# Kernel tuning notes

Measured on AMD Instinct MI355X. Metric: run time of the kernel, lower is better.

## Reference

```python
import jax, jax.numpy as jnp
import numpy as np
from jax import lax

B, L, E, H, VOCAB = 32, 64, 1024, 128, 32000


def setup_inputs() -> dict:
    key = jax.random.key(0)
    ks = jax.random.split(key, 8)
    return {
        "sent": jax.random.randint(ks[0], (B, L), 0, VOCAB),
        "init_c": jax.random.normal(ks[1], (B, H), jnp.float32),
        "init_h": jax.random.normal(ks[2], (B, H), jnp.float32),
        "enc_output": jax.random.normal(ks[3], (B, E, H), jnp.float32),
        "w_emb": jax.random.normal(ks[4], (VOCAB, H), jnp.float32) * 0.02,
        "w_lstm": jax.random.normal(ks[5], (2 * H, 4 * H), jnp.float32) * 0.05,
        "w_soft": jax.random.normal(ks[6], (H, VOCAB), jnp.float32) * 0.05,
        "V": jax.random.normal(ks[7], (2 * H, H), jnp.float32) * 0.05,
    }


def reference(sent, init_c, init_h, enc_output, w_emb, w_lstm, w_soft, V):
    h_dim = init_h.shape[-1]
    x_emb = w_emb[sent]                       # (B, L, H) embedding lookup
    # Split additive-attention matrix: concat(enc, h) @ V == enc @ V_e + h @ V_h
    V_e, V_h = V[:h_dim], V[h_dim:]           # (H, H) each
    enc_proj = enc_output @ V_e               # (B, E, H), precomputed once

    def step(carry, x_t):
        c, h = carry
        # LSTM cell: gates from concat(x, h) @ w_lstm
        gates = jnp.concatenate([x_t, h], axis=-1) @ w_lstm   # (B, 4H)
        i, f, o, g = jnp.split(gates, 4, axis=-1)
        c_new = jax.nn.sigmoid(f) * c + jax.nn.sigmoid(i) * jnp.tanh(g)
        h_new = jax.nn.sigmoid(o) * jnp.tanh(c_new)           # (B, H)
        # Bahdanau additive attention over encoder states
        att = jnp.tanh(enc_proj + (h_new @ V_h)[:, None, :])  # (B, E, H)
        scores = att.sum(axis=-1)                              # (B, E)
        alpha = jax.nn.softmax(scores, axis=-1)                # (B, E)
        context = jnp.einsum('be,beh->bh', alpha, enc_output)  # (B, H)
        h_out = context                                        # attended hidden
        return (c_new, h_out), (h_out, alpha)

    (c_fin, h_fin), (hs, alphas) = lax.scan(step, (init_c, init_h),
                                            jnp.transpose(x_emb, (1, 0, 2)))
    hs = jnp.transpose(hs, (1, 0, 2))          # (B, L, H)
    alphas = jnp.transpose(alphas, (1, 0, 2))  # (B, L, E)
    logits = hs @ w_soft                       # (B, L, vocab)
    return logits, c_fin, h_fin, alphas
```

## Files before the change

kernel.cpp:

```cpp
#include <hip/hip_runtime.h>
#include <hip/hip_bf16.h>

#define BB 32
#define LL 64
#define EE 1024
#define HH 128
#define VV 32000

typedef unsigned short u16;
typedef unsigned long long u64;
typedef __attribute__((ext_vector_type(8))) short bf16x8;
typedef __attribute__((ext_vector_type(4))) float f32x4;

#define LOG2E 1.4426950408889634f
#define C2T   2.8853900817779268f

#define OFF_C ((size_t)BB * LL * VV)
#define OFF_H (OFF_C + (size_t)BB * HH)
#define OFF_A (OFF_H + (size_t)BB * HH)

#define WS_ENCT 0
#define WS_HS   ((size_t)16777216)
#define WS_GX   ((size_t)18350080)
#define WS_PAYU ((size_t)22544384)
#define WS_PAYG ((size_t)23076864)
#define WS_DFL  ((size_t)23339008)
#define WS_NEED ((size_t)23339012)

#define PAYU_WORDS (32 * 8 * 2 * 130)
#define PAYG_WORDS (32 * 8 * 2 * 64)
#define PAY_TOTAL  (PAYU_WORDS + PAYG_WORDS)

__device__ __forceinline__ float bf2f(u16 u) {
    union { unsigned int i; float f; } v; v.i = ((unsigned int)u) << 16; return v.f;
}
__device__ __forceinline__ u16 f2bf(float f) {
    union { float f; unsigned int i; } v; v.f = f;
    unsigned int x = v.i;
    return (u16)((x + 0x7FFFu + ((x >> 16) & 1u)) >> 16);
}
__device__ __forceinline__ float ldf(const void* p, size_t i, int f32) {
    if (f32) return ((const float*)p)[i];
    return bf2f(((const u16*)p)[i]);
}
__device__ __forceinline__ void stout(void* p, size_t i, float v, int f32) {
    if (f32) ((float*)p)[i] = v;
    else ((u16*)p)[i] = f2bf(v);
}
__device__ __forceinline__ float sigm(float x) {
    return __builtin_amdgcn_rcpf(1.f + __builtin_amdgcn_exp2f(-x * LOG2E));
}
__device__ __forceinline__ float tanh_fast(float x) {
    return 1.f - 2.f * __builtin_amdgcn_rcpf(__builtin_amdgcn_exp2f(x * C2T) + 1.f);
}

__global__ __launch_bounds__(256) void resetdetect_kernel(
    u64* __restrict__ pay, const unsigned int* __restrict__ w, int* __restrict__ flag)
{
    int i = blockIdx.x * 256 + threadIdx.x;
    if (i < PAY_TOTAL)
        pay[i] = 0ull;
    if (i == 0) {
        int cnt = 0;
        for (int j = 0; j < 256; ++j) {
            float a = fabsf(bf2f((u16)(w[j] & 0xFFFFu)));
            if (a > 1e-4f && a < 0.5f) ++cnt;
        }
        *flag = (cnt > 128) ? 1 : 0;
    }
}

__global__ __launch_bounds__(256) void gatesx3_kernel(
    const int* __restrict__ sent, const void* __restrict__ w_emb,
    const void* __restrict__ w_lstm, float* __restrict__ gx,
    const int* __restrict__ flagp)
{
    int isf32 = !flagp[0];
    int row0 = blockIdx.x * 16;
    int tid = threadIdx.x;
    __shared__ float xr[16][128];
    for (int i = tid; i < 2048; i += 256) {
        int r = i >> 7, col = i & 127;
        int id = sent[row0 + r];
        xr[r][col] = ldf(w_emb, (size_t)id * HH + col, isf32);
    }
    __syncthreads();
    int c0 = tid, c1 = tid + 256;
    float a0[16], a1[16];
    #pragma unroll
    for (int r = 0; r < 16; ++r) { a0[r] = 0.f; a1[r] = 0.f; }
    for (int kk = 0; kk < 128; ++kk) {
        float w0, w1;
        if (isf32) {
            w0 = ((const float*)w_lstm)[(size_t)kk * 512 + c0];
            w1 = ((const float*)w_lstm)[(size_t)kk * 512 + c1];
        } else {
            w0 = bf2f(((const u16*)w_lstm)[(size_t)kk * 512 + c0]);
            w1 = bf2f(((const u16*)w_lstm)[(size_t)kk * 512 + c1]);
        }
        #pragma unroll
        for (int r = 0; r < 16; ++r) {
            a0[r] += xr[r][kk] * w0;
            a1[r] += xr[r][kk] * w1;
        }
    }
    #pragma unroll
    for (int r = 0; r < 16; ++r) {
        gx[(size_t)(row0 + r) * 512 + c0] = a0[r];
        gx[(size_t)(row0 + r) * 512 + c1] = a1[r];
    }
}

__global__ __launch_bounds__(1024) void transpose_wsoft(
    const void* __restrict__ w_soft, u16* __restrict__ wT, const int* __restrict__ flagp)
{
    int isf32 = !flagp[0];
    __shared__ u16 tile[32][33];
    int n0 = blockIdx.x * 32;
    int k0 = blockIdx.y * 32;
    int tx = threadIdx.x & 31, ty = threadIdx.x >> 5;
    tile[ty][tx] = f2bf(ldf(w_soft, (size_t)(k0 + ty) * VV + n0 + tx, isf32));
    __syncthreads();
    wT[(size_t)(n0 + ty) * HH + k0 + tx] = tile[tx][ty];
}

__global__ __launch_bounds__(256) void encproj_kernel(
    const void* __restrict__ enc_out, const void* __restrict__ V,
    float* __restrict__ encT, const int* __restrict__ flagp)
{
    int isf32 = !flagp[0];
    __shared__ float ve[HH][HH];
    int b = blockIdx.y;
    int e0 = blockIdx.x * 64;
    int tid = threadIdx.x;
    for (int i = tid; i < HH * HH; i += 256)
        ve[i >> 7][i & 127] = ldf(V, i, isf32);
    __syncthreads();
    int e = e0 + (tid & 63);
    int hb = (tid >> 6) * 32;
    size_t rowbase = ((size_t)b * EE + e) * HH;
    float acc[32];
    #pragma unroll
    for (int i = 0; i < 32; ++i) acc[i] = 0.f;
    for (int k0 = 0; k0 < HH; k0 += 16) {
        float ef[16];
        #pragma unroll
        for (int i = 0; i < 16; ++i) ef[i] = ldf(enc_out, rowbase + k0 + i, isf32);
        #pragma unroll
        for (int hh = 0; hh < 32; ++hh) {
            float a = acc[hh];
            #pragma unroll
            for (int kk = 0; kk < 16; ++kk)
                a += ef[kk] * ve[k0 + kk][hb + hh];
            acc[hh] = a;
        }
    }
    float* outp = encT + ((size_t)b * HH) * EE + e;
    #pragma unroll
    for (int hh = 0; hh < 32; ++hh)
        outp[(size_t)(hh + hb) * EE] = acc[hh] * C2T;
}

__global__ __launch_bounds__(1024) void scan_kernel(
    const void* __restrict__ init_c, const void* __restrict__ init_h,
    const void* __restrict__ enc_out, const void* __restrict__ w_lstm,
    const void* __restrict__ V, const float* __restrict__ encTg,
    const float* __restrict__ gx, u16* __restrict__ hs_bf,
    void* __restrict__ out, u64* __restrict__ payu, u64* __restrict__ payg,
    const int* __restrict__ flagp)
{
    const int isf32 = !flagp[0];
    const int bid = blockIdx.x;
    const int b = bid & 31, k = bid >> 5;
    const int tid = threadIdx.x;

    __shared__ u16   encTl16[128][128];
    __shared__ float encF[128][128];
    __shared__ u16   wrec16[64 * 128];
    __shared__ float gall[512];
    __shared__ float harr[128], cst[128], hnew[128], hvC[128];
    __shared__ float dred[8][128];
    __shared__ float sc[128];
    __shared__ float exch[8][130];
    __shared__ float redw[2], redw2[2];
    __shared__ float m_s, s_s;

    for (int i = tid; i < 128 * 128; i += 1024) {
        int h = i >> 7, e = i & 127;
        encTl16[h][e] = f2bf(encTg[(size_t)(b * 128 + h) * EE + k * 128 + e]);
    }
    for (int i = tid; i < 128 * 128; i += 1024) {
        int e = i >> 7, hh = i & 127;
        encF[e][hh] = ldf(enc_out, ((size_t)b * EE + k * 128 + e) * HH + hh, isf32);
    }
    for (int i = tid; i < 64 * 128; i += 1024) {
        int c = i >> 7, kk = i & 127;
        wrec16[c * 128 + kk] = f2bf(ldf(w_lstm, (size_t)(HH + kk) * 512 + k * 64 + c, isf32));
    }
    if (tid < 128) {
        cst[tid]  = ldf(init_c, (size_t)b * HH + tid, isf32);
        harr[tid] = ldf(init_h, (size_t)b * HH + tid, isf32);
    }
    __syncthreads();

    u64* mypu = payu + (size_t)(b * 8 + k) * 2 * 130;
    u64* mypg = payg + (size_t)(b * 8 + k) * 2 * 64;

    for (int t = 0; t < LL; ++t) {
        const unsigned int want = (unsigned int)(t + 1);
        float g0 = 0.f, g1 = 0.f, g2 = 0.f, g3 = 0.f;
        if (tid < 128) {
            const float* gxr = gx + (size_t)(b * LL + t) * 512;
            g0 = gxr[tid]; g1 = gxr[128 + tid]; g2 = gxr[256 + tid]; g3 = gxr[384 + tid];
        }
        {
            int colL = tid >> 4, kc = tid & 15;
            const bf16x8 wv = *(const bf16x8*)&wrec16[colL * 128 + kc * 8];
            float acc = 0.f;
            #pragma unroll
            for (int j = 0; j < 8; ++j)
                acc = __builtin_fmaf(harr[kc * 8 + j], bf2f((u16)wv[j]), acc);
            acc += __shfl_xor(acc, 1);
            acc += __shfl_xor(acc, 2);
            acc += __shfl_xor(acc, 4);
            acc += __shfl_xor(acc, 8);
            if (kc == 0) {
                gall[(k << 6) + colL] = acc;
                union { float f; unsigned int u; } cv; cv.f = acc;
                u64 w = ((u64)want << 32) | (u64)cv.u;
                __hip_atomic_store(&mypg[(size_t)(t & 1) * 64 + colL], w,
                                   __ATOMIC_RELAXED, __HIP_MEMORY_SCOPE_AGENT);
            }
        }
        if (tid < 448) {
            int qq = tid >> 6;
            int q = qq + (qq >= k ? 1 : 0);
            int idx = tid & 63;
            const u64* qp = payg + ((size_t)(b * 8 + q) * 2 + (t & 1)) * 64 + idx;
            u64 w = __hip_atomic_load(qp, __ATOMIC_RELAXED, __HIP_MEMORY_SCOPE_AGENT);
            int cnt = 0;
            while ((unsigned int)(w >> 32) != want) {
                __builtin_amdgcn_s_sleep(1);
                w = __hip_atomic_load(qp, __ATOMIC_RELAXED, __HIP_MEMORY_SCOPE_AGENT);
                if (++cnt > (1 << 20)) break;
            }
            union { unsigned int u; float f; } cv; cv.u = (unsigned int)(w & 0xFFFFFFFFu);
            gall[q * 64 + idx] = cv.f;
        }
        __syncthreads();
        if (tid < 128) {
            float gi = g0 + gall[tid];
            float gf = g1 + gall[128 + tid];
            float go = g2 + gall[256 + tid];
            float gg = g3 + gall[384 + tid];
            float c_new = sigm(gf) * cst[tid] + sigm(gi) * tanh_fast(gg);
            cst[tid] = c_new;
            hnew[tid] = sigm(go) * tanh_fast(c_new);
        }
        __syncthreads();
        {
            int h = tid & 127, jc = tid >> 7;
            float p = 0.f;
            if (isf32) {
                const float* vp = (const float*)V + (size_t)(HH + jc * 16) * HH + h;
                #pragma unroll
                for (int j = 0; j < 16; ++j)
                    p += hnew[jc * 16 + j] * vp[(size_t)j * HH];
            } else {
                const u16* vp = (const u16*)V + (size_t)(HH + jc * 16) * HH + h;
                #pragma unroll
                for (int j = 0; j < 16; ++j)
                    p += hnew[jc * 16 + j] * bf2f(vp[(size_t)j * HH]);
            }
            dred[jc][h] = p;
        }
        __syncthreads();
        if (tid < 128) {
            float v = 0.f;
            #pragma unroll
            for (int s = 0; s < 8; ++s) v += dred[s][tid];
            hvC[tid] = v * C2T;
        }
        __syncthreads();
        {
            int e = tid & 127, hc = tid >> 7;
            float sumr = 0.f;
            #pragma unroll
            for (int j = 0; j < 16; ++j) {
                int h = hc * 16 + j;
                float a = bf2f(encTl16[h][e]) + hvC[h];
                sumr += __builtin_amdgcn_rcpf(__builtin_amdgcn_exp2f(a) + 1.f);
            }
            dred[hc][e] = sumr;
        }
        __syncthreads();
        float s_e = 0.f, p_reg = 0.f;
        if (tid < 128) {
            float sr = 0.f;
            #pragma unroll
            for (int s = 0; s < 8; ++s) sr += dred[s][tid];
            s_e = 128.f - 2.f * sr;
            float m = s_e;
            #pragma unroll
            for (int off = 32; off; off >>= 1) m = fmaxf(m, __shfl_xor(m, off));
            if ((tid & 63) == 0) redw[tid >> 6] = m;
        }
        __syncthreads();
        if (tid < 128) {
            float mloc = fmaxf(redw[0], redw[1]);
            p_reg = __builtin_amdgcn_exp2f((s_e - mloc) * LOG2E);
            sc[tid] = p_reg;
            float s = p_reg;
            #pragma unroll
            for (int off = 32; off; off >>= 1) s += __shfl_xor(s, off);
            if ((tid & 63) == 0) redw2[tid >> 6] = s;
            if (tid == 0) m_s = mloc;
        }
        __syncthreads();
        if (tid == 0) s_s = redw2[0] + redw2[1];
        {
            int h = tid & 127, ec = tid >> 7;
            float p = 0.f;
            #pragma unroll
            for (int j = 0; j < 16; ++j)
                p += sc[ec * 16 + j] * encF[ec * 16 + j][h];
            dred[ec][h] = p;
        }
        __syncthreads();
        float Uv = 0.f;
        if (tid < 128) {
            #pragma unroll
            for (int s = 0; s < 8; ++s) Uv += dred[s][tid];
        }
        {
            u64* pp = mypu + (size_t)(t & 1) * 130;
            if (tid < 130) {
                float val = (tid < 128) ? Uv : ((tid == 128) ? m_s : s_s);
                union { float f; unsigned int u; } cv; cv.f = val;
                u64 w = ((u64)want << 32) | (u64)cv.u;
                __hip_atomic_store(&pp[tid], w, __ATOMIC_RELAXED, __HIP_MEMORY_SCOPE_AGENT);
                exch[k][tid] = val;
            }
        }
        if (tid < 910) {
            int qq = tid / 130;
            int q = qq + (qq >= k ? 1 : 0);
            int idx = tid - qq * 130;
            const u64* qp = payu + ((size_t)(b * 8 + q) * 2 + (t & 1)) * 130 + idx;
            u64 w = __hip_atomic_load(qp, __ATOMIC_RELAXED, __HIP_MEMORY_SCOPE_AGENT);
            int cnt = 0;
            while ((unsigned int)(w >> 32) != want) {
                __builtin_amdgcn_s_sleep(1);
                w = __hip_atomic_load(qp, __ATOMIC_RELAXED, __HIP_MEMORY_SCOPE_AGENT);
                if (++cnt > (1 << 20)) break;
            }
            union { unsigned int u; float f; } cv; cv.u = (unsigned int)(w & 0xFFFFFFFFu);
            exch[q][idx] = cv.f;
        }
        __syncthreads();
        if (tid < 128) {
            float M = exch[0][128];
            #pragma unroll
            for (int q = 1; q < 8; ++q) M = fmaxf(M, exch[q][128]);
            float St = 0.f, ch = 0.f;
            #pragma unroll
            for (int q = 0; q < 8; ++q) {
                float w = __builtin_amdgcn_exp2f((exch[q][128] - M) * LOG2E);
                St += w * exch[q][129];
                ch += w * exch[q][tid];
            }
            float rS = __builtin_amdgcn_rcpf(St);
            float ctx = ch * rS;
            harr[tid] = ctx;
            float al = p_reg * __builtin_amdgcn_exp2f((m_s - M) * LOG2E) * rS;
            stout(out, OFF_A + (size_t)(b * LL + t) * EE + k * 128 + tid, al, isf32);
            if (k == 0) {
                hs_bf[(size_t)(b * LL + t) * HH + tid] = f2bf(ctx);
                if (t == LL - 1) {
                    stout(out, OFF_H + (size_t)b * HH + tid, ctx, isf32);
                    stout(out, OFF_C + (size_t)b * HH + tid, cst[tid], isf32);
                }
            }
        }
        __syncthreads();
    }
}

__global__ __launch_bounds__(256) void logits_gemm(
    const u16* __restrict__ hs, const u16* __restrict__ wT,
    void* __restrict__ out, const int* __restrict__ flagp)
{
    int isf32 = !flagp[0];
    int n0 = blockIdx.x * 32;
    int m0 = (blockIdx.y * 4 + (threadIdx.x >> 6)) * 32;
    int lane = threadIdx.x & 63;
    int lr = lane & 15, lh = lane >> 4;
    f32x4 acc00 = {0.f, 0.f, 0.f, 0.f}, acc01 = acc00, acc10 = acc00, acc11 = acc00;
    const u16* a0p = hs + (size_t)(m0 + lr) * HH + lh * 8;
    const u16* a1p = a0p + (size_t)16 * HH;
    const u16* b0p = wT + (size_t)(n0 + lr) * HH + lh * 8;
    const u16* b1p = b0p + (size_t)16 * HH;
    #pragma unroll
    for (int ks = 0; ks < 4; ++ks) {
        bf16x8 a0 = *(const bf16x8*)(a0p + ks * 32);
        bf16x8 a1 = *(const bf16x8*)(a1p + ks * 32);
        bf16x8 b0 = *(const bf16x8*)(b0p + ks * 32);
        bf16x8 b1 = *(const bf16x8*)(b1p + ks * 32);
        acc00 = __builtin_amdgcn_mfma_f32_16x16x32_bf16(a0, b0, acc00, 0, 0, 0);
        acc01 = __builtin_amdgcn_mfma_f32_16x16x32_bf16(a0, b1, acc01, 0, 0, 0);
        acc10 = __builtin_amdgcn_mfma_f32_16x16x32_bf16(a1, b0, acc10, 0, 0, 0);
        acc11 = __builtin_amdgcn_mfma_f32_16x16x32_bf16(a1, b1, acc11, 0, 0, 0);
    }
    size_t base0 = (size_t)(m0 + lh * 4) * VV + n0;
    size_t base1 = (size_t)(m0 + 16 + lh * 4) * VV + n0;
    #pragma unroll
    for (int r = 0; r < 4; ++r) {
        stout(out, base0 + (size_t)r * VV + lr,      acc00[r], isf32);
        stout(out, base0 + (size_t)r * VV + 16 + lr, acc01[r], isf32);
        stout(out, base1 + (size_t)r * VV + lr,      acc10[r], isf32);
        stout(out, base1 + (size_t)r * VV + 16 + lr, acc11[r], isf32);
    }
}

extern "C" void kernel_launch(void* const* d_in, const int* in_sizes, int n_in,
                              void* d_out, int out_size, void* d_ws, size_t ws_size,
                              hipStream_t stream)
{
    (void)in_sizes; (void)n_in; (void)out_size;
    if (ws_size < WS_NEED) return;

    const int* sent     = (const int*)d_in[0];
    const void* init_c  = d_in[1];
    const void* init_h  = d_in[2];
    const void* enc_out = d_in[3];
    const void* w_emb   = d_in[4];
    const void* w_lstm  = d_in[5];
    const void* w_soft  = d_in[6];
    const void* V       = d_in[7];

    char* ws = (char*)d_ws;
    float* encT  = (float*)(ws + WS_ENCT);
    u16*   wT    = (u16*)(ws + WS_ENCT);
    u16*   hs    = (u16*)(ws + WS_HS);
    float* gx    = (float*)(ws + WS_GX);
    u64*   payu  = (u64*)(ws + WS_PAYU);
    u64*   payg  = (u64*)(ws + WS_PAYG);
    int*   dflag = (int*)(ws + WS_DFL);

    hipLaunchKernelGGL(resetdetect_kernel, dim3((PAY_TOTAL + 255) / 256), dim3(256), 0, stream,
                       payu, (const unsigned int*)w_emb, dflag);
    hipLaunchKernelGGL(gatesx3_kernel, dim3(128), dim3(256), 0, stream,
                       sent, w_emb, w_lstm, gx, dflag);
    hipLaunchKernelGGL(encproj_kernel, dim3(16, BB), dim3(256), 0, stream, enc_out, V, encT, dflag);

    {
        const void* a0 = init_c; const void* a1 = init_h; const void* a2 = enc_out;
        const void* a3 = w_lstm; const void* a4 = V; const float* a5 = encT;
        const float* a6 = gx; u16* a7 = hs; void* a8 = d_out;
        u64* a9 = payu; u64* a10 = payg; const int* a11 = dflag;
        void* args[] = {&a0, &a1, &a2, &a3, &a4, &a5, &a6, &a7, &a8, &a9, &a10, &a11};
        hipLaunchCooperativeKernel(scan_kernel, dim3(256), dim3(1024), args, 0, stream);
    }

    hipLaunchKernelGGL(transpose_wsoft, dim3(VV / 32, 4), dim3(1024), 0, stream, w_soft, wT, dflag);
    hipLaunchKernelGGL(logits_gemm, dim3(VV / 32, 16), dim3(256), 0, stream, hs, wT, d_out, dflag);
}
```

Before: 775.9 us.

## Compute full recurrent gate GEMV per block, drop cross-block gate exchange

```diff
diff --git a/kernel.cpp b/kernel.cpp
--- a/kernel.cpp
+++ b/kernel.cpp
@@ -10,6 +10,7 @@
 typedef unsigned short u16;
 typedef unsigned long long u64;
 typedef __attribute__((ext_vector_type(8))) short bf16x8;
+typedef __attribute__((ext_vector_type(8))) unsigned short u16x8;
 typedef __attribute__((ext_vector_type(4))) float f32x4;
 
 #define LOG2E 1.4426950408889634f
@@ -20,16 +21,15 @@
 #define OFF_A (OFF_H + (size_t)BB * HH)
 
 #define WS_ENCT 0
-#define WS_HS   ((size_t)16777216)
-#define WS_GX   ((size_t)18350080)
-#define WS_PAYU ((size_t)22544384)
-#define WS_PAYG ((size_t)23076864)
-#define WS_DFL  ((size_t)23339008)
-#define WS_NEED ((size_t)23339012)
+#define WS_WREC ((size_t)8388608)
+#define WS_HS   ((size_t)8519680)
+#define WS_GX   ((size_t)9043968)
+#define WS_PAYU ((size_t)13238272)
+#define WS_WT   ((size_t)13770752)
+#define WS_DFL  ((size_t)21962752)
+#define WS_NEED ((size_t)21962756)
 
 #define PAYU_WORDS (32 * 8 * 2 * 130)
-#define PAYG_WORDS (32 * 8 * 2 * 64)
-#define PAY_TOTAL  (PAYU_WORDS + PAYG_WORDS)
 
 __device__ __forceinline__ float bf2f(u16 u) {
     union { unsigned int i; float f; } v; v.i = ((unsigned int)u) << 16; return v.f;
@@ -58,7 +58,7 @@
     u64* __restrict__ pay, const unsigned int* __restrict__ w, int* __restrict__ flag)
 {
     int i = blockIdx.x * 256 + threadIdx.x;
-    if (i < PAY_TOTAL)
+    if (i < PAYU_WORDS)
         pay[i] = 0ull;
     if (i == 0) {
         int cnt = 0;
@@ -68,6 +68,19 @@
         }
         *flag = (cnt > 128) ? 1 : 0;
     }
+}
+
+__global__ __launch_bounds__(1024) void prep_wrec(
+    const void* __restrict__ w_lstm, u16* __restrict__ wrecT, const int* __restrict__ flagp)
+{
+    int isf32 = !flagp[0];
+    __shared__ u16 tile[32][33];
+    int c0 = blockIdx.x * 32;
+    int k0 = blockIdx.y * 32;
+    int tx = threadIdx.x & 31, ty = threadIdx.x >> 5;
+    tile[ty][tx] = f2bf(ldf(w_lstm, (size_t)(HH + k0 + ty) * 512 + c0 + tx, isf32));
+    __syncthreads();
+    wrecT[(size_t)(c0 + ty) * 128 + k0 + tx] = tile[tx][ty];
 }
 
 __global__ __launch_bounds__(256) void gatesx3_kernel(
@@ -126,7 +139,7 @@
 
 __global__ __launch_bounds__(256) void encproj_kernel(
     const void* __restrict__ enc_out, const void* __restrict__ V,
-    float* __restrict__ encT, const int* __restrict__ flagp)
+    u16* __restrict__ encT, const int* __restrict__ flagp)
 {
     int isf32 = !flagp[0];
     __shared__ float ve[HH][HH];
@@ -155,18 +168,18 @@
             acc[hh] = a;
         }
     }
-    float* outp = encT + ((size_t)b * HH) * EE + e;
+    u16* outp = encT + ((size_t)b * HH) * EE + e;
     #pragma unroll
     for (int hh = 0; hh < 32; ++hh)
-        outp[(size_t)(hh + hb) * EE] = acc[hh] * C2T;
+        outp[(size_t)(hh + hb) * EE] = f2bf(acc[hh] * C2T);
 }
 
 __global__ __launch_bounds__(1024) void scan_kernel(
     const void* __restrict__ init_c, const void* __restrict__ init_h,
-    const void* __restrict__ enc_out, const void* __restrict__ w_lstm,
-    const void* __restrict__ V, const float* __restrict__ encTg,
+    const void* __restrict__ enc_out, const u16* __restrict__ wrecT,
+    const void* __restrict__ V, const u16* __restrict__ encTg16,
     const float* __restrict__ gx, u16* __restrict__ hs_bf,
-    void* __restrict__ out, u64* __restrict__ payu, u64* __restrict__ payg,
+    void* __restrict__ out, u64* __restrict__ payu,
     const int* __restrict__ flagp)
 {
     const int isf32 = !flagp[0];
@@ -174,10 +187,8 @@
     const int b = bid & 31, k = bid >> 5;
     const int tid = threadIdx.x;
 
-    __shared__ u16   encTl16[128][128];
-    __shared__ float encF[128][128];
-    __shared__ u16   wrec16[64 * 128];
-    __shared__ float gall[512];
+    __shared__ u16   wrecl[512 * 128];
+    __shared__ float gp[512];
     __shared__ float harr[128], cst[128], hnew[128], hvC[128];
     __shared__ float dred[8][128];
     __shared__ float sc[128];
@@ -185,18 +196,8 @@
     __shared__ float redw[2], redw2[2];
     __shared__ float m_s, s_s;
 
-    for (int i = tid; i < 128 * 128; i += 1024) {
-        int h = i >> 7, e = i & 127;
-        encTl16[h][e] = f2bf(encTg[(size_t)(b * 128 + h) * EE + k * 128 + e]);
-    }
-    for (int i = tid; i < 128 * 128; i += 1024) {
-        int e = i >> 7, hh = i & 127;
-        encF[e][hh] = ldf(enc_out, ((size_t)b * EE + k * 128 + e) * HH + hh, isf32);
-    }
-    for (int i = tid; i < 64 * 128; i += 1024) {
-        int c = i >> 7, kk = i & 127;
-        wrec16[c * 128 + kk] = f2bf(ldf(w_lstm, (size_t)(HH + kk) * 512 + k * 64 + c, isf32));
-    }
+    for (int i = tid; i < 8192; i += 1024)
+        *(u16x8*)&wrecl[i * 8] = *(const u16x8*)&wrecT[(size_t)i * 8];
     if (tid < 128) {
         cst[tid]  = ldf(init_c, (size_t)b * HH + tid, isf32);
         harr[tid] = ldf(init_h, (size_t)b * HH + tid, isf32);
@@ -204,7 +205,6 @@
     __syncthreads();
 
     u64* mypu = payu + (size_t)(b * 8 + k) * 2 * 130;
-    u64* mypg = payg + (size_t)(b * 8 + k) * 2 * 64;
 
     for (int t = 0; t < LL; ++t) {
         const unsigned int want = (unsigned int)(t + 1);
@@ -214,45 +214,28 @@
             g0 = gxr[tid]; g1 = gxr[128 + tid]; g2 = gxr[256 + tid]; g3 = gxr[384 + tid];
         }
         {
-            int colL = tid >> 4, kc = tid & 15;
-            const bf16x8 wv = *(const bf16x8*)&wrec16[colL * 128 + kc * 8];
-            float acc = 0.f;
-            #pragma unroll
-            for (int j = 0; j < 8; ++j)
-                acc = __builtin_fmaf(harr[kc * 8 + j], bf2f((u16)wv[j]), acc);
-            acc += __shfl_xor(acc, 1);
-            acc += __shfl_xor(acc, 2);
-            acc += __shfl_xor(acc, 4);
-            acc += __shfl_xor(acc, 8);
-            if (kc == 0) {
-                gall[(k << 6) + colL] = acc;
-                union { float f; unsigned int u; } cv; cv.f = acc;
-                u64 w = ((u64)want << 32) | (u64)cv.u;
-                __hip_atomic_store(&mypg[(size_t)(t & 1) * 64 + colL], w,
-                                   __ATOMIC_RELAXED, __HIP_MEMORY_SCOPE_AGENT);
-            }
-        }
-        if (tid < 448) {
-            int qq = tid >> 6;
-            int q = qq + (qq >= k ? 1 : 0);
-            int idx = tid & 63;
-            const u64* qp = payg + ((size_t)(b * 8 + q) * 2 + (t & 1)) * 64 + idx;
-            u64 w = __hip_atomic_load(qp, __ATOMIC_RELAXED, __HIP_MEMORY_SCOPE_AGENT);
-            int cnt = 0;
-            while ((unsigned int)(w >> 32) != want) {
-                __builtin_amdgcn_s_sleep(1);
-                w = __hip_atomic_load(qp, __ATOMIC_RELAXED, __HIP_MEMORY_SCOPE_AGENT);
-                if (++cnt > (1 << 20)) break;
-            }
-            union { unsigned int u; float f; } cv; cv.u = (unsigned int)(w & 0xFFFFFFFFu);
-            gall[q * 64 + idx] = cv.f;
-        }
-        __syncthreads();
-        if (tid < 128) {
-            float gi = g0 + gall[tid];
-            float gf = g1 + gall[128 + tid];
-            float go = g2 + gall[256 + tid];
-            float gg = g3 + gall[384 + tid];
+            int kc = tid & 15, colb = tid >> 4;
+            #pragma unroll
+            for (int it = 0; it < 8; ++it) {
+                int col = colb + (it << 6);
+                const bf16x8 wv = *(const bf16x8*)&wrecl[col * 128 + kc * 8];
+                float acc = 0.f;
+                #pragma unroll
+                for (int j = 0; j < 8; ++j)
+                    acc = __builtin_fmaf(harr[kc * 8 + j], bf2f((u16)wv[j]), acc);
+                acc += __shfl_xor(acc, 1);
+                acc += __shfl_xor(acc, 2);
+                acc += __shfl_xor(acc, 4);
+                acc += __shfl_xor(acc, 8);
+                if (kc == 0) gp[col] = acc;
+            }
+        }
+        __syncthreads();
+        if (tid < 128) {
+            float gi = g0 + gp[tid];
+            float gf = g1 + gp[128 + tid];
+            float go = g2 + gp[256 + tid];
+            float gg = g3 + gp[384 + tid];
             float c_new = sigm(gf) * cst[tid] + sigm(gi) * tanh_fast(gg);
             cst[tid] = c_new;
             hnew[tid] = sigm(go) * tanh_fast(c_new);
@@ -284,11 +267,11 @@
         __syncthreads();
         {
             int e = tid & 127, hc = tid >> 7;
+            const u16* ep = encTg16 + (size_t)(b * 128 + hc * 16) * EE + k * 128 + e;
             float sumr = 0.f;
             #pragma unroll
             for (int j = 0; j < 16; ++j) {
-                int h = hc * 16 + j;
-                float a = bf2f(encTl16[h][e]) + hvC[h];
+                float a = bf2f(ep[(size_t)j * EE]) + hvC[hc * 16 + j];
                 sumr += __builtin_amdgcn_rcpf(__builtin_amdgcn_exp2f(a) + 1.f);
             }
             dred[hc][e] = sumr;
@@ -321,9 +304,19 @@
         {
             int h = tid & 127, ec = tid >> 7;
             float p = 0.f;
-            #pragma unroll
-            for (int j = 0; j < 16; ++j)
-                p += sc[ec * 16 + j] * encF[ec * 16 + j][h];
+            if (isf32) {
+                const float* eb = (const float*)enc_out +
+                    ((size_t)b * EE + k * 128 + ec * 16) * HH + h;
+                #pragma unroll
+                for (int j = 0; j < 16; ++j)
+                    p += sc[ec * 16 + j] * eb[(size_t)j * HH];
+            } else {
+                const u16* eb = (const u16*)enc_out +
+                    ((size_t)b * EE + k * 128 + ec * 16) * HH + h;
+                #pragma unroll
+                for (int j = 0; j < 16; ++j)
+                    p += sc[ec * 16 + j] * bf2f(eb[(size_t)j * HH]);
+            }
             dred[ec][h] = p;
         }
         __syncthreads();
@@ -439,26 +432,27 @@
     const void* V       = d_in[7];
 
     char* ws = (char*)d_ws;
-    float* encT  = (float*)(ws + WS_ENCT);
-    u16*   wT    = (u16*)(ws + WS_ENCT);
+    u16*   encT  = (u16*)(ws + WS_ENCT);
+    u16*   wrecT = (u16*)(ws + WS_WREC);
     u16*   hs    = (u16*)(ws + WS_HS);
     float* gx    = (float*)(ws + WS_GX);
     u64*   payu  = (u64*)(ws + WS_PAYU);
-    u64*   payg  = (u64*)(ws + WS_PAYG);
+    u16*   wT    = (u16*)(ws + WS_WT);
     int*   dflag = (int*)(ws + WS_DFL);
 
-    hipLaunchKernelGGL(resetdetect_kernel, dim3((PAY_TOTAL + 255) / 256), dim3(256), 0, stream,
+    hipLaunchKernelGGL(resetdetect_kernel, dim3((PAYU_WORDS + 255) / 256), dim3(256), 0, stream,
                        payu, (const unsigned int*)w_emb, dflag);
+    hipLaunchKernelGGL(prep_wrec, dim3(16, 4), dim3(1024), 0, stream, w_lstm, wrecT, dflag);
     hipLaunchKernelGGL(gatesx3_kernel, dim3(128), dim3(256), 0, stream,
                        sent, w_emb, w_lstm, gx, dflag);
     hipLaunchKernelGGL(encproj_kernel, dim3(16, BB), dim3(256), 0, stream, enc_out, V, encT, dflag);
 
     {
         const void* a0 = init_c; const void* a1 = init_h; const void* a2 = enc_out;
-        const void* a3 = w_lstm; const void* a4 = V; const float* a5 = encT;
+        const u16* a3 = wrecT; const void* a4 = V; const u16* a5 = encT;
         const float* a6 = gx; u16* a7 = hs; void* a8 = d_out;
-        u64* a9 = payu; u64* a10 = payg; const int* a11 = dflag;
-        void* args[] = {&a0, &a1, &a2, &a3, &a4, &a5, &a6, &a7, &a8, &a9, &a10, &a11};
+        u64* a9 = payu; const int* a10 = dflag;
+        void* args[] = {&a0, &a1, &a2, &a3, &a4, &a5, &a6, &a7, &a8, &a9, &a10};
         hipLaunchCooperativeKernel(scan_kernel, dim3(256), dim3(1024), args, 0, stream);
     }
 
```

Measured after the change: 807.5 us. +4.1%, slower.

## Replace shared-memory reductions with wave shuffles and store enc projection as bf16

Applied to the files above, without the earlier changes.

```diff
diff --git a/kernel.cpp b/kernel.cpp
--- a/kernel.cpp
+++ b/kernel.cpp
@@ -10,6 +10,7 @@
 typedef unsigned short u16;
 typedef unsigned long long u64;
 typedef __attribute__((ext_vector_type(8))) short bf16x8;
+typedef __attribute__((ext_vector_type(8))) unsigned short u16x8;
 typedef __attribute__((ext_vector_type(4))) float f32x4;
 
 #define LOG2E 1.4426950408889634f
@@ -20,12 +21,13 @@
 #define OFF_A (OFF_H + (size_t)BB * HH)
 
 #define WS_ENCT 0
-#define WS_HS   ((size_t)16777216)
-#define WS_GX   ((size_t)18350080)
-#define WS_PAYU ((size_t)22544384)
-#define WS_PAYG ((size_t)23076864)
-#define WS_DFL  ((size_t)23339008)
-#define WS_NEED ((size_t)23339012)
+#define WS_HS   ((size_t)8388608)
+#define WS_GX   ((size_t)8912896)
+#define WS_PAYU ((size_t)13107200)
+#define WS_PAYG ((size_t)13639680)
+#define WS_WT   ((size_t)13901824)
+#define WS_DFL  ((size_t)22093824)
+#define WS_NEED ((size_t)22093828)
 
 #define PAYU_WORDS (32 * 8 * 2 * 130)
 #define PAYG_WORDS (32 * 8 * 2 * 64)
@@ -126,7 +128,7 @@
 
 __global__ __launch_bounds__(256) void encproj_kernel(
     const void* __restrict__ enc_out, const void* __restrict__ V,
-    float* __restrict__ encT, const int* __restrict__ flagp)
+    u16* __restrict__ encT, const int* __restrict__ flagp)
 {
     int isf32 = !flagp[0];
     __shared__ float ve[HH][HH];
@@ -155,16 +157,16 @@
             acc[hh] = a;
         }
     }
-    float* outp = encT + ((size_t)b * HH) * EE + e;
+    u16* outp = encT + ((size_t)b * EE + e) * HH;
     #pragma unroll
     for (int hh = 0; hh < 32; ++hh)
-        outp[(size_t)(hh + hb) * EE] = acc[hh] * C2T;
+        outp[hb + hh] = f2bf(acc[hh] * C2T);
 }
 
 __global__ __launch_bounds__(1024) void scan_kernel(
     const void* __restrict__ init_c, const void* __restrict__ init_h,
     const void* __restrict__ enc_out, const void* __restrict__ w_lstm,
-    const void* __restrict__ V, const float* __restrict__ encTg,
+    const void* __restrict__ V, const u16* __restrict__ encTg16,
     const float* __restrict__ gx, u16* __restrict__ hs_bf,
     void* __restrict__ out, u64* __restrict__ payu, u64* __restrict__ payg,
     const int* __restrict__ flagp)
@@ -173,25 +175,25 @@
     const int bid = blockIdx.x;
     const int b = bid & 31, k = bid >> 5;
     const int tid = threadIdx.x;
-
-    __shared__ u16   encTl16[128][128];
-    __shared__ float encF[128][128];
+    const int w = tid >> 6;
+    const int l = tid & 63;
+
     __shared__ u16   wrec16[64 * 128];
+    __shared__ u16   encTl[128][136];
+    __shared__ float encF[128][132];
     __shared__ float gall[512];
     __shared__ float harr[128], cst[128], hnew[128], hvC[128];
-    __shared__ float dred[8][128];
     __shared__ float sc[128];
-    __shared__ float exch[8][130];
-    __shared__ float redw[2], redw2[2];
-    __shared__ float m_s, s_s;
+    __shared__ float pairs[16][2];
+    __shared__ float exch[8][132];
 
     for (int i = tid; i < 128 * 128; i += 1024) {
-        int h = i >> 7, e = i & 127;
-        encTl16[h][e] = f2bf(encTg[(size_t)(b * 128 + h) * EE + k * 128 + e]);
+        int e = i >> 7, h = i & 127;
+        encTl[e][h] = encTg16[((size_t)b * EE + k * 128 + e) * HH + h];
     }
     for (int i = tid; i < 128 * 128; i += 1024) {
-        int e = i >> 7, hh = i & 127;
-        encF[e][hh] = ldf(enc_out, ((size_t)b * EE + k * 128 + e) * HH + hh, isf32);
+        int e = i >> 7, h = i & 127;
+        encF[e][h] = ldf(enc_out, ((size_t)b * EE + k * 128 + e) * HH + h, isf32);
     }
     for (int i = tid; i < 64 * 128; i += 1024) {
         int c = i >> 7, kk = i & 127;
@@ -227,8 +229,8 @@
             if (kc == 0) {
                 gall[(k << 6) + colL] = acc;
                 union { float f; unsigned int u; } cv; cv.f = acc;
-                u64 w = ((u64)want << 32) | (u64)cv.u;
-                __hip_atomic_store(&mypg[(size_t)(t & 1) * 64 + colL], w,
+                u64 wd = ((u64)want << 32) | (u64)cv.u;
+                __hip_atomic_store(&mypg[(size_t)(t & 1) * 64 + colL], wd,
                                    __ATOMIC_RELAXED, __HIP_MEMORY_SCOPE_AGENT);
             }
         }
@@ -237,14 +239,14 @@
             int q = qq + (qq >= k ? 1 : 0);
             int idx = tid & 63;
             const u64* qp = payg + ((size_t)(b * 8 + q) * 2 + (t & 1)) * 64 + idx;
-            u64 w = __hip_atomic_load(qp, __ATOMIC_RELAXED, __HIP_MEMORY_SCOPE_AGENT);
+            u64 wd = __hip_atomic_load(qp, __ATOMIC_RELAXED, __HIP_MEMORY_SCOPE_AGENT);
             int cnt = 0;
-            while ((unsigned int)(w >> 32) != want) {
+            while ((unsigned int)(wd >> 32) != want) {
                 __builtin_amdgcn_s_sleep(1);
-                w = __hip_atomic_load(qp, __ATOMIC_RELAXED, __HIP_MEMORY_SCOPE_AGENT);
+                wd = __hip_atomic_load(qp, __ATOMIC_RELAXED, __HIP_MEMORY_SCOPE_AGENT);
                 if (++cnt > (1 << 20)) break;
             }
-            union { unsigned int u; float f; } cv; cv.u = (unsigned int)(w & 0xFFFFFFFFu);
+            union { unsigned int u; float f; } cv; cv.u = (unsigned int)(wd & 0xFFFFFFFFu);
             gall[q * 64 + idx] = cv.f;
         }
         __syncthreads();
@@ -259,87 +261,103 @@
         }
         __syncthreads();
         {
-            int h = tid & 127, jc = tid >> 7;
+            int r = l >> 3, c = l & 7;
+            int h = 8 * w + r;
             float p = 0.f;
             if (isf32) {
-                const float* vp = (const float*)V + (size_t)(HH + jc * 16) * HH + h;
+                const float* vp = (const float*)V + (size_t)(HH + 16 * c) * HH + h;
                 #pragma unroll
                 for (int j = 0; j < 16; ++j)
-                    p += hnew[jc * 16 + j] * vp[(size_t)j * HH];
+                    p += hnew[16 * c + j] * vp[(size_t)j * HH];
             } else {
-                const u16* vp = (const u16*)V + (size_t)(HH + jc * 16) * HH + h;
+                const u16* vp = (const u16*)V + (size_t)(HH + 16 * c) * HH + h;
                 #pragma unroll
                 for (int j = 0; j < 16; ++j)
-                    p += hnew[jc * 16 + j] * bf2f(vp[(size_t)j * HH]);
-            }
-            dred[jc][h] = p;
-        }
-        __syncthreads();
-        if (tid < 128) {
-            float v = 0.f;
-            #pragma unroll
-            for (int s = 0; s < 8; ++s) v += dred[s][tid];
-            hvC[tid] = v * C2T;
-        }
-        __syncthreads();
+                    p += hnew[16 * c + j] * bf2f(vp[(size_t)j * HH]);
+            }
+            p += __shfl_xor(p, 1);
+            p += __shfl_xor(p, 2);
+            p += __shfl_xor(p, 4);
+            if (c == 0) hvC[h] = p * C2T;
+        }
+        __syncthreads();
+        float s_e, m_loc, S_loc;
         {
-            int e = tid & 127, hc = tid >> 7;
+            int r = l >> 3, c = l & 7;
+            int e = 8 * w + r;
+            const u16* ep = &encTl[e][16 * c];
+            bf16x8 v0 = *(const bf16x8*)ep;
+            bf16x8 v1 = *(const bf16x8*)(ep + 8);
             float sumr = 0.f;
             #pragma unroll
+            for (int j = 0; j < 8; ++j) {
+                float a = bf2f((u16)v0[j]) + hvC[16 * c + j];
+                sumr += __builtin_amdgcn_rcpf(__builtin_amdgcn_exp2f(a) + 1.f);
+            }
+            #pragma unroll
+            for (int j = 0; j < 8; ++j) {
+                float a = bf2f((u16)v1[j]) + hvC[16 * c + 8 + j];
+                sumr += __builtin_amdgcn_rcpf(__builtin_amdgcn_exp2f(a) + 1.f);
+            }
+            sumr += __shfl_xor(sumr, 1);
+            sumr += __shfl_xor(sumr, 2);
+            sumr += __shfl_xor(sumr, 4);
+            s_e = 128.f - 2.f * sumr;
+            float m = s_e;
+            m = fmaxf(m, __shfl_xor(m, 8));
+            m = fmaxf(m, __shfl_xor(m, 16));
+            m = fmaxf(m, __shfl_xor(m, 32));
+            float pw = __builtin_amdgcn_exp2f((s_e - m) * LOG2E);
+            float Sw = pw;
+            Sw += __shfl_xor(Sw, 8);
+            Sw += __shfl_xor(Sw, 16);
+            Sw += __shfl_xor(Sw, 32);
+            if (l == 0) { pairs[w][0] = m; pairs[w][1] = Sw; }
+        }
+        __syncthreads();
+        {
+            m_loc = pairs[0][0];
+            #pragma unroll
+            for (int q = 1; q < 16; ++q) m_loc = fmaxf(m_loc, pairs[q][0]);
+            S_loc = 0.f;
+            #pragma unroll
+            for (int q = 0; q < 16; ++q)
+                S_loc += pairs[q][1] * __builtin_amdgcn_exp2f((pairs[q][0] - m_loc) * LOG2E);
+            int r = l >> 3, c = l & 7;
+            float p_e = __builtin_amdgcn_exp2f((s_e - m_loc) * LOG2E);
+            if (c == 0) sc[8 * w + r] = p_e;
+        }
+        __syncthreads();
+        {
+            int r = l >> 3, c = l & 7;
+            int h = 8 * w + r;
+            float U = 0.f;
+            #pragma unroll
             for (int j = 0; j < 16; ++j) {
-                int h = hc * 16 + j;
-                float a = bf2f(encTl16[h][e]) + hvC[h];
-                sumr += __builtin_amdgcn_rcpf(__builtin_amdgcn_exp2f(a) + 1.f);
-            }
-            dred[hc][e] = sumr;
-        }
-        __syncthreads();
-        float s_e = 0.f, p_reg = 0.f;
-        if (tid < 128) {
-            float sr = 0.f;
-            #pragma unroll
-            for (int s = 0; s < 8; ++s) sr += dred[s][tid];
-            s_e = 128.f - 2.f * sr;
-            float m = s_e;
-            #pragma unroll
-            for (int off = 32; off; off >>= 1) m = fmaxf(m, __shfl_xor(m, off));
-            if ((tid & 63) == 0) redw[tid >> 6] = m;
-        }
-        __syncthreads();
-        if (tid < 128) {
-            float mloc = fmaxf(redw[0], redw[1]);
-            p_reg = __builtin_amdgcn_exp2f((s_e - mloc) * LOG2E);
-            sc[tid] = p_reg;
-            float s = p_reg;
-            #pragma unroll
-            for (int off = 32; off; off >>= 1) s += __shfl_xor(s, off);
-            if ((tid & 63) == 0) redw2[tid >> 6] = s;
-            if (tid == 0) m_s = mloc;
-        }
-        __syncthreads();
-        if (tid == 0) s_s = redw2[0] + redw2[1];
-        {
-            int h = tid & 127, ec = tid >> 7;
-            float p = 0.f;
-            #pragma unroll
-            for (int j = 0; j < 16; ++j)
-                p += sc[ec * 16 + j] * encF[ec * 16 + j][h];
-            dred[ec][h] = p;
-        }
-        __syncthreads();
-        float Uv = 0.f;
-        if (tid < 128) {
-            #pragma unroll
-            for (int s = 0; s < 8; ++s) Uv += dred[s][tid];
-        }
-        {
+                int e = 8 * j + c;
+                U = __builtin_fmaf(sc[e], encF[e][h], U);
+            }
+            U += __shfl_xor(U, 1);
+            U += __shfl_xor(U, 2);
+            U += __shfl_xor(U, 4);
             u64* pp = mypu + (size_t)(t & 1) * 130;
-            if (tid < 130) {
-                float val = (tid < 128) ? Uv : ((tid == 128) ? m_s : s_s);
-                union { float f; unsigned int u; } cv; cv.f = val;
-                u64 w = ((u64)want << 32) | (u64)cv.u;
-                __hip_atomic_store(&pp[tid], w, __ATOMIC_RELAXED, __HIP_MEMORY_SCOPE_AGENT);
-                exch[k][tid] = val;
+            if (c == 0) {
+                union { float f; unsigned int u; } cv; cv.f = U;
+                u64 wd = ((u64)want << 32) | (u64)cv.u;
+                __hip_atomic_store(&pp[h], wd, __ATOMIC_RELAXED, __HIP_MEMORY_SCOPE_AGENT);
+                exch[k][h] = U;
+            }
+            if (tid == 128) {
+                union { float f; unsigned int u; } cv; cv.f = m_loc;
+                u64 wd = ((u64)want << 32) | (u64)cv.u;
+                __hip_atomic_store(&pp[128], wd, __ATOMIC_RELAXED, __HIP_MEMORY_SCOPE_AGENT);
+                exch[k][128] = m_loc;
+            }
+            if (tid == 129) {
+                union { float f; unsigned int u; } cv; cv.f = S_loc;
+                u64 wd = ((u64)want << 32) | (u64)cv.u;
+                __hip_atomic_store(&pp[129], wd, __ATOMIC_RELAXED, __HIP_MEMORY_SCOPE_AGENT);
+                exch[k][129] = S_loc;
             }
         }
         if (tid < 910) {
@@ -347,14 +365,14 @@
             int q = qq + (qq >= k ? 1 : 0);
             int idx = tid - qq * 130;
             const u64* qp = payu + ((size_t)(b * 8 + q) * 2 + (t & 1)) * 130 + idx;
-            u64 w = __hip_atomic_load(qp, __ATOMIC_RELAXED, __HIP_MEMORY_SCOPE_AGENT);
+            u64 wd = __hip_atomic_load(qp, __ATOMIC_RELAXED, __HIP_MEMORY_SCOPE_AGENT);
             int cnt = 0;
-            while ((unsigned int)(w >> 32) != want) {
+            while ((unsigned int)(wd >> 32) != want) {
                 __builtin_amdgcn_s_sleep(1);
-                w = __hip_atomic_load(qp, __ATOMIC_RELAXED, __HIP_MEMORY_SCOPE_AGENT);
+                wd = __hip_atomic_load(qp, __ATOMIC_RELAXED, __HIP_MEMORY_SCOPE_AGENT);
                 if (++cnt > (1 << 20)) break;
             }
-            union { unsigned int u; float f; } cv; cv.u = (unsigned int)(w & 0xFFFFFFFFu);
+            union { unsigned int u; float f; } cv; cv.u = (unsigned int)(wd & 0xFFFFFFFFu);
             exch[q][idx] = cv.f;
         }
         __syncthreads();
@@ -365,14 +383,14 @@
             float St = 0.f, ch = 0.f;
             #pragma unroll
             for (int q = 0; q < 8; ++q) {
-                float w = __builtin_amdgcn_exp2f((exch[q][128] - M) * LOG2E);
-                St += w * exch[q][129];
-                ch += w * exch[q][tid];
+                float wq = __builtin_amdgcn_exp2f((exch[q][128] - M) * LOG2E);
+                St += wq * exch[q][129];
+                ch += wq * exch[q][tid];
             }
             float rS = __builtin_amdgcn_rcpf(St);
             float ctx = ch * rS;
             harr[tid] = ctx;
-            float al = p_reg * __builtin_amdgcn_exp2f((m_s - M) * LOG2E) * rS;
+            float al = sc[tid] * __builtin_amdgcn_exp2f((m_loc - M) * LOG2E) * rS;
             stout(out, OFF_A + (size_t)(b * LL + t) * EE + k * 128 + tid, al, isf32);
             if (k == 0) {
                 hs_bf[(size_t)(b * LL + t) * HH + tid] = f2bf(ctx);
@@ -439,12 +457,12 @@
     const void* V       = d_in[7];
 
     char* ws = (char*)d_ws;
-    float* encT  = (float*)(ws + WS_ENCT);
-    u16*   wT    = (u16*)(ws + WS_ENCT);
+    u16*   encT  = (u16*)(ws + WS_ENCT);
     u16*   hs    = (u16*)(ws + WS_HS);
     float* gx    = (float*)(ws + WS_GX);
     u64*   payu  = (u64*)(ws + WS_PAYU);
     u64*   payg  = (u64*)(ws + WS_PAYG);
+    u16*   wT    = (u16*)(ws + WS_WT);
     int*   dflag = (int*)(ws + WS_DFL);
 
     hipLaunchKernelGGL(resetdetect_kernel, dim3((PAY_TOTAL + 255) / 256), dim3(256), 0, stream,
@@ -455,7 +473,7 @@
 
     {
         const void* a0 = init_c; const void* a1 = init_h; const void* a2 = enc_out;
-        const void* a3 = w_lstm; const void* a4 = V; const float* a5 = encT;
+        const void* a3 = w_lstm; const void* a4 = V; const u16* a5 = encT;
         const float* a6 = gx; u16* a7 = hs; void* a8 = d_out;
         u64* a9 = payu; u64* a10 = payg; const int* a11 = dflag;
         void* args[] = {&a0, &a1, &a2, &a3, &a4, &a5, &a6, &a7, &a8, &a9, &a10, &a11};
```

After: 1.004 ms. 29.3% more time.
